# Performance work log

Measured on AMD Instinct MI355X. Metric: run time of the kernel, lower is better.

The kernel has to match this reference:

```python
import jax, jax.numpy as jnp
import numpy as np

EMBED = 1024
HEADS = 16
HEAD_DIM = EMBED // HEADS


def setup_inputs() -> dict:
    key = jax.random.key(0)
    ks = jax.random.split(key, 9)
    s = 1.0 / np.sqrt(EMBED)
    return {
        "embeddings": jax.random.normal(ks[0], (4, 2048, EMBED), dtype=jnp.float32),
        "wq": jax.random.uniform(ks[1], (EMBED, EMBED), jnp.float32, -s, s),
        "bq": jax.random.uniform(ks[2], (EMBED,), jnp.float32, -s, s),
        "wk": jax.random.uniform(ks[3], (EMBED, EMBED), jnp.float32, -s, s),
        "bk": jax.random.uniform(ks[4], (EMBED,), jnp.float32, -s, s),
        "wv": jax.random.uniform(ks[5], (EMBED, EMBED), jnp.float32, -s, s),
        "bv": jax.random.uniform(ks[6], (EMBED,), jnp.float32, -s, s),
        "wo": jax.random.uniform(ks[7], (EMBED, EMBED), jnp.float32, -s, s),
        "bo": jax.random.uniform(ks[8], (EMBED,), jnp.float32, -s, s),
    }


def reference(embeddings, wq, bq, wk, bk, wv, bv, wo, bo):
    b, s, _ = embeddings.shape
    # Projections: x @ W^T + b (torch nn.Linear convention)
    q = (embeddings @ wq.T + bq).reshape(b, s, HEADS, HEAD_DIM)
    k = (embeddings @ wk.T + bk).reshape(b, s, HEADS, HEAD_DIM)
    v = (embeddings @ wv.T + bv).reshape(b, s, HEADS, HEAD_DIM)
    scale = 1.0 / np.sqrt(HEAD_DIM).astype(np.float32)
    # scores: [b, h, s, s]
    scores = jnp.einsum("bqhd,bkhd->bhqk", q, k) * scale
    probs = jax.nn.softmax(scores, axis=-1)
    attn = jnp.einsum("bhqk,bkhd->bqhd", probs, v).reshape(b, s, EMBED)
    return attn @ wo.T + bo
```

## Files before the change

kernel.cpp:

```cpp
#include <hip/hip_runtime.h>
#include <hip/hip_bf16.h>
#include <math.h>

using bf16x8 = __attribute__((ext_vector_type(8))) short;
using f32x4  = __attribute__((ext_vector_type(4))) float;
using f32x16 = __attribute__((ext_vector_type(16))) float;
using i32x4  = __attribute__((ext_vector_type(4))) int;
using i32x2  = __attribute__((ext_vector_type(2))) int;

#define MFMA32(a, b, c) __builtin_amdgcn_mfma_f32_32x32x16_bf16((a), (b), (c), 0, 0, 0)

__device__ __forceinline__ float bf2f(short s) {
    union { unsigned u; float f; } v;
    v.u = ((unsigned)(unsigned short)s) << 16;
    return v.f;
}
__device__ __forceinline__ short f2bf(float f) {
    union { float f; unsigned u; } v; v.f = f;
    unsigned r = v.u + 0x7FFF + ((v.u >> 16) & 1);
    return (short)(r >> 16);
}
__device__ __forceinline__ int cvtpk_bf16(float lo, float hi) {
    int r;
    asm("v_cvt_pk_bf16_f32 %0, %1, %2" : "=v"(r) : "v"(lo), "v"(hi));
    return r;
}
__device__ __forceinline__ void permswap(int &a, int &b) {
#if __has_builtin(__builtin_amdgcn_permlane32_swap)
    typedef unsigned u32x2v __attribute__((ext_vector_type(2)));
    u32x2v r = __builtin_amdgcn_permlane32_swap((unsigned)a, (unsigned)b, false, false);
    a = (int)r[0]; b = (int)r[1];
#else
    asm volatile("v_permlane32_swap_b32 %0, %1" : "+v"(a), "+v"(b));
#endif
}
__device__ __forceinline__ float fexp2(float x) {
#if __has_builtin(__builtin_amdgcn_exp2f)
    return __builtin_amdgcn_exp2f(x);
#else
    return exp2f(x);
#endif
}

__device__ __forceinline__ void gload_lds16(const void* g, void* l) {
    __builtin_amdgcn_global_load_lds(
        (const __attribute__((address_space(1))) void*)g,
        (__attribute__((address_space(3))) void*)l, 16, 0, 0);
}

__global__ void preprocess(
    const void* __restrict__ emb, short* __restrict__ embC,
    const void* __restrict__ w0, const void* __restrict__ w1,
    const void* __restrict__ w2, const void* __restrict__ w3,
    const void* __restrict__ b0, const void* __restrict__ b1,
    const void* __restrict__ b2, const void* __restrict__ b3,
    short* dw0, short* dw1, short* dw2, short* dw3,
    short* db0, short* db1, short* db2, short* db3,
    int* flagp)
{
    __shared__ int vote;
    const int tid = threadIdx.x;
    if (tid == 0) vote = 0;
    __syncthreads();
    {
        unsigned short v = ((const unsigned short*)emb)[2 * tid];
        unsigned e = (v >> 7) & 0xFF;
        int c = (v == 0 || v == 0x8000u || (e >= 97 && e <= 137)) ? 1 : 0;
        atomicAdd(&vote, c);
    }
    __syncthreads();
    const int fl = vote > 128;
    if (blockIdx.x == 0 && tid == 0) *flagp = fl;

    const void* src; short* dst; int idx;
    if (blockIdx.x < 4096) {
        src = emb; dst = embC; idx = blockIdx.x * 256 + tid;
    } else {
        int i = (blockIdx.x - 4096) * 256 + tid;
        if (i < 524288) {
            int w = i >> 17; idx = i & 131071;
            src = (w == 0) ? w0 : (w == 1) ? w1 : (w == 2) ? w2 : w3;
            dst = (w == 0) ? dw0 : (w == 1) ? dw1 : (w == 2) ? dw2 : dw3;
        } else {
            int j = i - 524288; int b = j >> 7; idx = j & 127;
            src = (b == 0) ? b0 : (b == 1) ? b1 : (b == 2) ? b2 : b3;
            dst = (b == 0) ? db0 : (b == 1) ? db1 : (b == 2) ? db2 : db3;
        }
    }
    if (fl) {
        ((bf16x8*)dst)[idx] = ((const bf16x8*)src)[idx];
    } else {
        const float* f = (const float*)src + (size_t)idx * 8;
        bf16x8 o;
#pragma unroll
        for (int j = 0; j < 8; j++) o[j] = f2bf(f[j]);
        ((bf16x8*)dst)[idx] = o;
    }
}

__global__ __launch_bounds__(512) void gemm256(
    const short* __restrict__ A,
    const short* __restrict__ B0, const short* __restrict__ B1,
    const short* __restrict__ B2,
    const short* __restrict__ bias0, const short* __restrict__ bias1,
    const short* __restrict__ bias2,
    void* __restrict__ C0, void* __restrict__ C1, void* __restrict__ C2,
    float s0, float s1, float s2,
    int mode0, int mode1, int mode2,
    const int* __restrict__ flag)
{
    constexpr int M = 8192, N = 1024, Kd = 1024, BK = 64;
    __shared__ __align__(16) short Al[2][256][BK];
    __shared__ __align__(16) short Bl[2][128][BK];

    const int z = blockIdx.z;
    const short* B    = (z == 0) ? B0    : (z == 1) ? B1    : B2;
    const short* bias = (z == 0) ? bias0 : (z == 1) ? bias1 : bias2;
    void*  C     = (z == 0) ? C0 : (z == 1) ? C1 : C2;
    float  scale = (z == 0) ? s0 : (z == 1) ? s1 : s2;
    int    mode  = (z == 0) ? mode0 : (z == 1) ? mode1 : mode2;

    const int tid  = threadIdx.x;
    const int lane = tid & 63;
    const int wave = tid >> 6;
    const int l31  = lane & 31;
    const int hi   = lane >> 5;
    const int xr   = (l31 & 7) ^ ((l31 >> 3) & 3);

    const int bid = blockIdx.x;
    const int swz = ((bid & 7) << 5) | (bid >> 3);
    const int m0 = (swz >> 3) * 256;
    const int n0 = (swz & 7) * 128;
    const int wm = (wave >> 1) * 64;
    const int wn = (wave & 1) * 64;

    const int sr  = lane >> 3;
    const int scb = (lane & 7) ^ sr;

    int fl = 1;
    if (mode == 2) fl = *flag;

    f32x16 acc[2][2];
#pragma unroll
    for (int i = 0; i < 2; i++)
#pragma unroll
        for (int j = 0; j < 2; j++)
#pragma unroll
            for (int r = 0; r < 16; r++) acc[i][j][r] = 0.f;

    auto stage = [&](int bufi, int k) {
#pragma unroll
        for (int t = 0; t < 4; t++) {
            const int r0 = wave * 32 + t * 8;
            gload_lds16(A + (size_t)(m0 + r0 + sr) * Kd + k + ((scb ^ t) & 7) * 8,
                        &Al[bufi][r0][0]);
        }
#pragma unroll
        for (int t = 0; t < 2; t++) {
            const int r0 = wave * 16 + t * 8;
            const int tb = (wave * 2 + t) & 3;
            gload_lds16(B + (size_t)(n0 + r0 + sr) * Kd + k + ((scb ^ tb) & 7) * 8,
                        &Bl[bufi][r0][0]);
        }
    };

    stage(0, 0);
    for (int k0 = 0; k0 < Kd; k0 += BK) {
        const int cur = (k0 >> 6) & 1;
        stage(cur ^ 1, (k0 + BK) & (Kd - 1));
        asm volatile("s_waitcnt vmcnt(6)" ::: "memory");
        __builtin_amdgcn_s_barrier();
        __builtin_amdgcn_sched_barrier(0);

#pragma unroll
        for (int ks = 0; ks < 4; ks++) {
            const int rc = (((ks << 1) | hi) ^ xr) * 8;
            bf16x8 a0 = *(const bf16x8*)(&Al[cur][wm + l31][rc]);
            bf16x8 a1 = *(const bf16x8*)(&Al[cur][wm + 32 + l31][rc]);
            bf16x8 b0 = *(const bf16x8*)(&Bl[cur][wn + l31][rc]);
            bf16x8 b1 = *(const bf16x8*)(&Bl[cur][wn + 32 + l31][rc]);
            acc[0][0] = MFMA32(a0, b0, acc[0][0]);
            acc[0][1] = MFMA32(a0, b1, acc[0][1]);
            acc[1][0] = MFMA32(a1, b0, acc[1][0]);
            acc[1][1] = MFMA32(a1, b1, acc[1][1]);
        }

        asm volatile("s_waitcnt lgkmcnt(0)" ::: "memory");
        __builtin_amdgcn_sched_barrier(0);
        __builtin_amdgcn_s_barrier();
    }

    if (mode == 1) {
#pragma unroll
        for (int j = 0; j < 2; j++) {
            const int col = n0 + wn + j * 32 + l31;
            const float bv = bf2f(bias[col]);
#pragma unroll
            for (int i = 0; i < 2; i++) {
#pragma unroll
                for (int g = 0; g < 4; g++) {
                    const int row = m0 + wm + i * 32 + g * 8 + 4 * hi;
                    const float v0 = (acc[i][j][g * 4 + 0] + bv) * scale;
                    const float v1 = (acc[i][j][g * 4 + 1] + bv) * scale;
                    const float v2 = (acc[i][j][g * 4 + 2] + bv) * scale;
                    const float v3 = (acc[i][j][g * 4 + 3] + bv) * scale;
                    i32x2 dd;
                    dd[0] = cvtpk_bf16(v0, v1);
                    dd[1] = cvtpk_bf16(v2, v3);
                    *(i32x2*)((short*)C + (size_t)col * M + row) = dd;
                }
            }
        }
    } else {
#pragma unroll
        for (int j = 0; j < 2; j++) {
            const int col = n0 + wn + j * 32 + l31;
            const float bv = bf2f(bias[col]);
#pragma unroll
            for (int i = 0; i < 2; i++) {
#pragma unroll
                for (int r = 0; r < 16; r++) {
                    const int row = m0 + wm + i * 32 + (r & 3) + 8 * (r >> 2) + 4 * hi;
                    const float v = (acc[i][j][r] + bv) * scale;
                    if (mode == 0) ((short*)C)[(size_t)row * N + col] = f2bf(v);
                    else {
                        if (fl) ((short*)C)[(size_t)row * N + col] = f2bf(v);
                        else    ((float*)C)[(size_t)row * N + col] = v;
                    }
                }
            }
        }
    }
}

__global__ __launch_bounds__(256) void attn_kernel(
    const short* Q, const short* __restrict__ K,
    const short* __restrict__ Vt, short* Aout)
{
    __shared__ __align__(16) short lds[2][2][64][64];

    const int tid  = threadIdx.x;
    const int lane = tid & 63;
    const int wave = tid >> 6;
    const int l31  = lane & 31;
    const int hi   = lane >> 5;
    const int xr   = (l31 & 7) ^ ((l31 >> 3) & 3);

    const int qt = blockIdx.x;
    const int bh = blockIdx.y;
    const int b  = bh >> 4, h = bh & 15;
    const int q0 = b * 2048 + qt * 128 + wave * 32;
    const int c0 = h * 64;

    const int sr  = lane >> 3;
    const int scb = (lane & 7) ^ sr;
    const int sarr = wave >> 1;

    const short* Kb = K  + (size_t)(b * 2048) * 1024 + c0;
    const short* Vb = Vt + (size_t)c0 * 8192 + b * 2048;

    bf16x8 qf[4];
#pragma unroll
    for (int slot = 0; slot < 4; slot++)
        qf[slot] = *(const bf16x8*)(Q + (size_t)(q0 + l31) * 1024 + c0 + slot * 16 + hi * 8);

    auto stage = [&](int bufi, int kt) {
#pragma unroll
        for (int t = 0; t < 4; t++) {
            const int r0 = ((wave & 1) * 4 + t) * 8;
            const int sc = (scb ^ t) * 8;
            short* dst = &lds[bufi][sarr][r0][0];
            if (sarr == 0)
                gload_lds16(Kb + (size_t)(kt + r0 + sr) * 1024 + sc, dst);
            else
                gload_lds16(Vb + (size_t)(r0 + sr) * 8192 + kt + sc, dst);
        }
    };

    bf16x8 onesf;
#pragma unroll
    for (int j = 0; j < 8; j++) onesf[j] = (short)0x3F80;

    f32x16 o[2], l_acc, fz;
#pragma unroll
    for (int r = 0; r < 16; r++) {
        o[0][r] = 0.f; o[1][r] = 0.f; l_acc[r] = 0.f; fz[r] = 0.f;
    }

    stage(0, 0);
    for (int kt = 0; kt < 2048; kt += 64) {
        const int cur = (kt >> 6) & 1;
        stage(cur ^ 1, (kt + 64) & 2047);
        asm volatile("s_waitcnt vmcnt(4)" ::: "memory");
        __builtin_amdgcn_s_barrier();
        __builtin_amdgcn_sched_barrier(0);

        f32x16 st[2];
#pragma unroll
        for (int blk = 0; blk < 2; blk++) {
#pragma unroll
            for (int slot = 0; slot < 4; slot++) {
                bf16x8 kf = *(const bf16x8*)
                    &lds[cur][0][blk * 32 + l31][(((slot << 1) | hi) ^ xr) * 8];
                st[blk] = (slot == 0) ? MFMA32(kf, qf[0], fz)
                                      : MFMA32(kf, qf[slot], st[blk]);
            }
        }

#pragma unroll
        for (int blk = 0; blk < 2; blk++)
#pragma unroll
            for (int r = 0; r < 16; r++)
                st[blk][r] = fexp2(st[blk][r]);

#pragma unroll
        for (int ks = 0; ks < 4; ks++) {
            const int blk = ks >> 1;
            const int rb  = (ks & 1) * 8;
            int A0 = cvtpk_bf16(st[blk][rb + 0], st[blk][rb + 1]);
            int A1 = cvtpk_bf16(st[blk][rb + 2], st[blk][rb + 3]);
            int B0 = cvtpk_bf16(st[blk][rb + 4], st[blk][rb + 5]);
            int B1 = cvtpk_bf16(st[blk][rb + 6], st[blk][rb + 7]);
            permswap(A0, B0);
            permswap(A1, B1);
            i32x4 paw; paw[0] = A0; paw[1] = A1; paw[2] = B0; paw[3] = B1;
            const bf16x8 pf = *(const bf16x8*)&paw;
            l_acc = MFMA32(pf, onesf, l_acc);
#pragma unroll
            for (int dblk = 0; dblk < 2; dblk++) {
                bf16x8 vf = *(const bf16x8*)
                    &lds[cur][1][dblk * 32 + l31][(((ks << 1) | hi) ^ xr) * 8];
                o[dblk] = MFMA32(pf, vf, o[dblk]);
            }
        }

        asm volatile("s_waitcnt lgkmcnt(0)" ::: "memory");
        __builtin_amdgcn_sched_barrier(0);
        __builtin_amdgcn_s_barrier();
    }

#pragma unroll
    for (int r = 0; r < 16; r++) {
        const int qrow = (r & 3) + 8 * (r >> 2) + 4 * hi;
        const float inv = 1.f / l_acc[r];
#pragma unroll
        for (int dblk = 0; dblk < 2; dblk++)
            Aout[(size_t)(q0 + qrow) * 1024 + c0 + dblk * 32 + l31] =
                f2bf(o[dblk][r] * inv);
    }
}

extern "C" void kernel_launch(void* const* d_in, const int* in_sizes, int n_in,
                              void* d_out, int out_size, void* d_ws, size_t ws_size,
                              hipStream_t stream)
{
    const size_t MB = (size_t)1024 * 1024;
    char* ws = (char*)d_ws;

    int*   flagp = (int*)ws;
    short* embC  = (short*)(ws + 1 * MB);
    short* wC[4] = { (short*)(ws + 17 * MB), (short*)(ws + 19 * MB),
                     (short*)(ws + 21 * MB), (short*)(ws + 23 * MB) };
    short* bC[4] = { (short*)(ws + 25 * MB), (short*)(ws + 25 * MB + 4096),
                     (short*)(ws + 25 * MB + 8192), (short*)(ws + 25 * MB + 12288) };

    short *Qb, *Kb, *Vt, *Ab;
    if (ws_size >= 90 * MB) {
        Qb = (short*)(ws + 26 * MB);
        Kb = (short*)(ws + 42 * MB);
        Vt = (short*)(ws + 58 * MB);
        Ab = (short*)(ws + 74 * MB);
    } else {
        Qb = (short*)(ws + 26 * MB);
        Kb = (short*)d_out;
        Vt = (short*)(ws + 42 * MB);
        Ab = Qb;
    }

    preprocess<<<6146, 256, 0, stream>>>(
        d_in[0], embC,
        d_in[1], d_in[3], d_in[5], d_in[7],
        d_in[2], d_in[4], d_in[6], d_in[8],
        wC[0], wC[1], wC[2], wC[3],
        bC[0], bC[1], bC[2], bC[3], flagp);

    dim3 blk(512);
    gemm256<<<dim3(256, 1, 3), blk, 0, stream>>>(
        embC, wC[0], wC[1], wC[2], bC[0], bC[1], bC[2],
        Qb, Kb, Vt, 0.18033688011112042f, 1.0f, 1.0f, 0, 0, 1, nullptr);

    attn_kernel<<<dim3(16, 64), dim3(256), 0, stream>>>(Qb, Kb, Vt, Ab);

    gemm256<<<dim3(256, 1, 1), blk, 0, stream>>>(
        Ab, wC[3], nullptr, nullptr, bC[3], nullptr, nullptr,
        d_out, nullptr, nullptr, 1.0f, 0.f, 0.f, 2, 0, 0, flagp);
}
```

Measured before the change: 296.0 us.

## Split GEMM K-step into two phases interleaving B staging with LDS reads

The projection GEMM main loop now issues the next A tile load before computing and defers the B tile load to the middle of the iteration. Each BK step is split into two half-steps: LDS fragments are loaded in bulk, then MFMAs run under raised wave priority (s_setprio). The goal is to overlap global-to-LDS traffic with MFMA work and to give the matrix core priority across waves. In exchange it adds an extra barrier per iteration, and the B buffer is written while other waves may still be reading cur, which relies on barrier ordering for correctness. The attention kernel also swaps a shared zero accumulator for an explicit per-block zero init, a minor register cleanup.

```diff
diff --git a/kernel.cpp b/kernel.cpp
--- a/kernel.cpp
+++ b/kernel.cpp
@@ -148,13 +148,15 @@
 #pragma unroll
             for (int r = 0; r < 16; r++) acc[i][j][r] = 0.f;
 
-    auto stage = [&](int bufi, int k) {
+    auto stageA = [&](int bufi, int k) {
 #pragma unroll
         for (int t = 0; t < 4; t++) {
             const int r0 = wave * 32 + t * 8;
             gload_lds16(A + (size_t)(m0 + r0 + sr) * Kd + k + ((scb ^ t) & 7) * 8,
                         &Al[bufi][r0][0]);
         }
+    };
+    auto stageB = [&](int bufi, int k) {
 #pragma unroll
         for (int t = 0; t < 2; t++) {
             const int r0 = wave * 16 + t * 8;
@@ -164,29 +166,60 @@
         }
     };
 
-    stage(0, 0);
+    stageA(0, 0);
+    stageB(0, 0);
     for (int k0 = 0; k0 < Kd; k0 += BK) {
         const int cur = (k0 >> 6) & 1;
-        stage(cur ^ 1, (k0 + BK) & (Kd - 1));
-        asm volatile("s_waitcnt vmcnt(6)" ::: "memory");
+        const int kn  = (k0 + BK) & (Kd - 1);
+
+        stageA(cur ^ 1, kn);
+        asm volatile("s_waitcnt vmcnt(4)" ::: "memory");
         __builtin_amdgcn_s_barrier();
         __builtin_amdgcn_sched_barrier(0);
 
-#pragma unroll
-        for (int ks = 0; ks < 4; ks++) {
+        bf16x8 a0[2], a1[2], b0[2], b1[2];
+#pragma unroll
+        for (int ks = 0; ks < 2; ks++) {
             const int rc = (((ks << 1) | hi) ^ xr) * 8;
-            bf16x8 a0 = *(const bf16x8*)(&Al[cur][wm + l31][rc]);
-            bf16x8 a1 = *(const bf16x8*)(&Al[cur][wm + 32 + l31][rc]);
-            bf16x8 b0 = *(const bf16x8*)(&Bl[cur][wn + l31][rc]);
-            bf16x8 b1 = *(const bf16x8*)(&Bl[cur][wn + 32 + l31][rc]);
-            acc[0][0] = MFMA32(a0, b0, acc[0][0]);
-            acc[0][1] = MFMA32(a0, b1, acc[0][1]);
-            acc[1][0] = MFMA32(a1, b0, acc[1][0]);
-            acc[1][1] = MFMA32(a1, b1, acc[1][1]);
-        }
-
+            a0[ks] = *(const bf16x8*)(&Al[cur][wm + l31][rc]);
+            a1[ks] = *(const bf16x8*)(&Al[cur][wm + 32 + l31][rc]);
+            b0[ks] = *(const bf16x8*)(&Bl[cur][wn + l31][rc]);
+            b1[ks] = *(const bf16x8*)(&Bl[cur][wn + 32 + l31][rc]);
+        }
         asm volatile("s_waitcnt lgkmcnt(0)" ::: "memory");
         __builtin_amdgcn_sched_barrier(0);
+        __builtin_amdgcn_s_setprio(1);
+#pragma unroll
+        for (int ks = 0; ks < 2; ks++) {
+            acc[0][0] = MFMA32(a0[ks], b0[ks], acc[0][0]);
+            acc[0][1] = MFMA32(a0[ks], b1[ks], acc[0][1]);
+            acc[1][0] = MFMA32(a1[ks], b0[ks], acc[1][0]);
+            acc[1][1] = MFMA32(a1[ks], b1[ks], acc[1][1]);
+        }
+        __builtin_amdgcn_s_setprio(0);
+        __builtin_amdgcn_s_barrier();
+
+#pragma unroll
+        for (int ks = 0; ks < 2; ks++) {
+            const int rc = ((((ks + 2) << 1) | hi) ^ xr) * 8;
+            a0[ks] = *(const bf16x8*)(&Al[cur][wm + l31][rc]);
+            a1[ks] = *(const bf16x8*)(&Al[cur][wm + 32 + l31][rc]);
+            b0[ks] = *(const bf16x8*)(&Bl[cur][wn + l31][rc]);
+            b1[ks] = *(const bf16x8*)(&Bl[cur][wn + 32 + l31][rc]);
+        }
+        stageB(cur ^ 1, kn);
+        __builtin_amdgcn_s_barrier();
+        asm volatile("s_waitcnt lgkmcnt(0)" ::: "memory");
+        __builtin_amdgcn_sched_barrier(0);
+        __builtin_amdgcn_s_setprio(1);
+#pragma unroll
+        for (int ks = 0; ks < 2; ks++) {
+            acc[0][0] = MFMA32(a0[ks], b0[ks], acc[0][0]);
+            acc[0][1] = MFMA32(a0[ks], b1[ks], acc[0][1]);
+            acc[1][0] = MFMA32(a1[ks], b0[ks], acc[1][0]);
+            acc[1][1] = MFMA32(a1[ks], b1[ks], acc[1][1]);
+        }
+        __builtin_amdgcn_s_setprio(0);
         __builtin_amdgcn_s_barrier();
     }
 
@@ -281,11 +314,9 @@
 #pragma unroll
     for (int j = 0; j < 8; j++) onesf[j] = (short)0x3F80;
 
-    f32x16 o[2], l_acc, fz;
-#pragma unroll
-    for (int r = 0; r < 16; r++) {
-        o[0][r] = 0.f; o[1][r] = 0.f; l_acc[r] = 0.f; fz[r] = 0.f;
-    }
+    f32x16 o[2], l_acc;
+#pragma unroll
+    for (int r = 0; r < 16; r++) { o[0][r] = 0.f; o[1][r] = 0.f; l_acc[r] = 0.f; }
 
     stage(0, 0);
     for (int kt = 0; kt < 2048; kt += 64) {
@@ -299,11 +330,12 @@
 #pragma unroll
         for (int blk = 0; blk < 2; blk++) {
 #pragma unroll
+            for (int r = 0; r < 16; r++) st[blk][r] = 0.f;
+#pragma unroll
             for (int slot = 0; slot < 4; slot++) {
                 bf16x8 kf = *(const bf16x8*)
                     &lds[cur][0][blk * 32 + l31][(((slot << 1) | hi) ^ xr) * 8];
-                st[blk] = (slot == 0) ? MFMA32(kf, qf[0], fz)
-                                      : MFMA32(kf, qf[slot], st[blk]);
+                st[blk] = MFMA32(kf, qf[slot], st[blk]);
             }
         }
 
```

Result: no change. 294.7 us (-0.5%).
